# Optimization experiments

Measured on AMD Instinct MI355X. Metric: run time of the kernel, lower is better.

Reference implementation:

```python
import jax, jax.numpy as jnp
import numpy as np

NB1, NB2, B1 = 4, 4, 48
IN_F, OUT_F = 4096, 4096
BATCH = 16384


def setup_inputs() -> dict:
    key = jax.random.key(0)
    k1, k2, k3, k4 = jax.random.split(key, 4)
    i = IN_F // NB1          # 1024, per-block input width
    l = OUT_F // NB2         # 1024, per-block output width
    x = jax.random.normal(k1, (BATCH, IN_F), jnp.float32)
    # kaiming-uniform-ish scale for the factors
    w1_bfly = jax.random.normal(k2, (NB1, NB2 * B1, i), jnp.float32) * (1.0 / np.sqrt(i))
    w2_bfly = jax.random.normal(k3, (NB2, l, NB1 * B1), jnp.float32) * (1.0 / np.sqrt(NB1 * B1))
    bias = jax.random.normal(k4, (OUT_F,), jnp.float32) * 0.01
    return {"x": x, "w1_bfly": w1_bfly, "w2_bfly": w2_bfly, "bias": bias}


def reference(x, w1_bfly, w2_bfly, bias):
    # blockdiag_butterfly_multiply_einsum (Monarch-style, two block-diagonal GEMMs)
    k, q, p = w1_bfly.shape   # k = nblocks1, q = nblocks2*b1, p = in/nblocks1
    l, s, r = w2_bfly.shape   # l = nblocks2, s = out/nblocks2, r = nblocks1*b1
    b1 = q // l
    batch = x.shape[0]
    xr = x.reshape(batch, k, p)
    # stage 1: block-diagonal matmul over nblocks1
    out1 = jnp.einsum('bkp,kqp->bkq', xr, w1_bfly)               # (b, k, l*b1)
    # block transpose: (b, k, (l b1)) -> (b, l, (k b1))
    out1 = out1.reshape(batch, k, l, b1).transpose(0, 2, 1, 3).reshape(batch, l, k * b1)
    # stage 2: block-diagonal matmul over nblocks2
    out2 = jnp.einsum('blr,lsr->bls', out1, w2_bfly)             # (b, l, s)
    return out2.reshape(batch, l * s) + bias
```

## Files before the change

### kernel.cpp

```cpp
#include <hip/hip_runtime.h>
#include <cstdint>
#include <cstddef>

typedef __attribute__((ext_vector_type(8))) short short8;
typedef __attribute__((ext_vector_type(4))) float f32x4;
typedef __attribute__((ext_vector_type(4))) short short4v;

__device__ __forceinline__ unsigned short f2bf(float f) {
  unsigned u = __builtin_bit_cast(unsigned, f);
  u += 0x7fffu + ((u >> 16) & 1u);
  return (unsigned short)(u >> 16);
}

__global__ __launch_bounds__(256) void cvt_k(const float* __restrict__ src,
                                             unsigned short* __restrict__ dst, int n) {
  int i = (blockIdx.x * 256 + threadIdx.x) * 4;
  if (i + 3 < n) {
    float4 v = *(const float4*)(src + i);
    short4v o;
    o.x = (short)f2bf(v.x); o.y = (short)f2bf(v.y);
    o.z = (short)f2bf(v.z); o.w = (short)f2bf(v.w);
    *(short4v*)(dst + i) = o;
  }
}

#define S1_LDA 72
__global__ __launch_bounds__(256) void stage1_k(
    const float* __restrict__ x, const unsigned short* __restrict__ w1bf,
    unsigned short* __restrict__ Y) {
  __shared__ __attribute__((aligned(16))) unsigned short As[128 * S1_LDA];
  __shared__ __attribute__((aligned(16))) unsigned short Bs[192 * S1_LDA];
  const int t  = threadIdx.x;
  const int r0 = blockIdx.x * 128;
  const int kb = blockIdx.y;

  const int lane = t & 63;
  const int w  = t >> 6;
  const int wm = w & 1, wn = w >> 1;
  const int lm = lane & 15;
  const int lk = lane >> 4;

  const int ar = t >> 1;
  const int ac = (t & 1) * 32;
  const float* xp = x + (size_t)(r0 + ar) * 4096 + kb * 1024 + ac;
  unsigned short* asp = &As[ar * S1_LDA + ac];

  f32x4 acc[4][6];
#pragma unroll
  for (int i = 0; i < 4; ++i)
#pragma unroll
    for (int j = 0; j < 6; ++j) acc[i][j] = (f32x4)0.0f;

  for (int kt = 0; kt < 16; ++kt) {
    float4 v[8];
    const float* xq = xp + kt * 64;
#pragma unroll
    for (int i = 0; i < 8; ++i) v[i] = *(const float4*)(xq + i * 4);
#pragma unroll
    for (int i = 0; i < 4; ++i) {
      float4 a0 = v[2 * i], a1 = v[2 * i + 1];
      short8 o;
      o[0] = (short)f2bf(a0.x); o[1] = (short)f2bf(a0.y);
      o[2] = (short)f2bf(a0.z); o[3] = (short)f2bf(a0.w);
      o[4] = (short)f2bf(a1.x); o[5] = (short)f2bf(a1.y);
      o[6] = (short)f2bf(a1.z); o[7] = (short)f2bf(a1.w);
      *(short8*)(asp + i * 8) = o;
    }
#pragma unroll
    for (int i = 0; i < 6; ++i) {
      int c = t + 256 * i;
      int br = c >> 3, bs = c & 7;
      const uint4* gsrc = (const uint4*)(w1bf + (size_t)(kb * 192 + br) * 1024 + kt * 64 + bs * 8);
      *(uint4*)&Bs[br * S1_LDA + bs * 8] = *gsrc;
    }
    __syncthreads();
#pragma unroll
    for (int ks = 0; ks < 2; ++ks) {
      const int ko = ks * 32 + lk * 8;
      short8 a[4], b[6];
#pragma unroll
      for (int rt = 0; rt < 4; ++rt)
        a[rt] = *(const short8*)&As[(wm * 64 + rt * 16 + lm) * S1_LDA + ko];
#pragma unroll
      for (int ct = 0; ct < 6; ++ct)
        b[ct] = *(const short8*)&Bs[(wn * 96 + ct * 16 + lm) * S1_LDA + ko];
#pragma unroll
      for (int rt = 0; rt < 4; ++rt)
#pragma unroll
        for (int ct = 0; ct < 6; ++ct)
          acc[rt][ct] = __builtin_amdgcn_mfma_f32_16x16x32_bf16(a[rt], b[ct], acc[rt][ct], 0, 0, 0);
    }
    __syncthreads();
  }

#pragma unroll
  for (int rt = 0; rt < 4; ++rt) {
#pragma unroll
    for (int ct = 0; ct < 6; ++ct) {
      int q  = wn * 96 + ct * 16 + lm;
      int li = q / 48, j = q - li * 48;
      size_t base = (size_t)(r0 + wm * 64 + rt * 16 + lk * 4) * 768 + li * 192 + kb * 48 + j;
#pragma unroll
      for (int reg = 0; reg < 4; ++reg)
        Y[base + (size_t)reg * 768] = f2bf(acc[rt][ct][reg]);
    }
  }
}

#define S2_LDA 104
__global__ __launch_bounds__(256) void stage2_k(
    const unsigned short* __restrict__ Y, const unsigned short* __restrict__ w2bf,
    const float* __restrict__ bias, float* __restrict__ out) {
  __shared__ __attribute__((aligned(16))) unsigned short As[128 * S2_LDA];
  __shared__ __attribute__((aligned(16))) unsigned short Bs[128 * S2_LDA];
  const int t  = threadIdx.x;
  const int n0 = blockIdx.x * 128;
  const int r0 = blockIdx.y * 128;
  const int l  = blockIdx.z;

  const int lane = t & 63;
  const int w  = t >> 6;
  const int wm = w & 1, wn = w >> 1;
  const int lm = lane & 15;
  const int lk = lane >> 4;

  f32x4 acc[4][4];
#pragma unroll
  for (int i = 0; i < 4; ++i)
#pragma unroll
    for (int j = 0; j < 4; ++j) acc[i][j] = (f32x4)0.0f;

  for (int kt = 0; kt < 2; ++kt) {
#pragma unroll
    for (int i = 0; i < 6; ++i) {
      int c = t + 256 * i;
      int row = c / 12, s = c - row * 12;
      const uint4* ga = (const uint4*)(Y + (size_t)(r0 + row) * 768 + l * 192 + kt * 96 + s * 8);
      *(uint4*)&As[row * S2_LDA + s * 8] = *ga;
      const uint4* gb = (const uint4*)(w2bf + (size_t)(l * 1024 + n0 + row) * 192 + kt * 96 + s * 8);
      *(uint4*)&Bs[row * S2_LDA + s * 8] = *gb;
    }
    __syncthreads();
#pragma unroll
    for (int ks = 0; ks < 3; ++ks) {
      const int ko = ks * 32 + lk * 8;
      short8 a[4], b[4];
#pragma unroll
      for (int rt = 0; rt < 4; ++rt)
        a[rt] = *(const short8*)&As[(wm * 64 + rt * 16 + lm) * S2_LDA + ko];
#pragma unroll
      for (int ct = 0; ct < 4; ++ct)
        b[ct] = *(const short8*)&Bs[(wn * 64 + ct * 16 + lm) * S2_LDA + ko];
#pragma unroll
      for (int rt = 0; rt < 4; ++rt)
#pragma unroll
        for (int ct = 0; ct < 4; ++ct)
          acc[rt][ct] = __builtin_amdgcn_mfma_f32_16x16x32_bf16(a[rt], b[ct], acc[rt][ct], 0, 0, 0);
    }
    __syncthreads();
  }

  float bv[4];
#pragma unroll
  for (int ct = 0; ct < 4; ++ct)
    bv[ct] = bias[l * 1024 + n0 + wn * 64 + ct * 16 + lm];
#pragma unroll
  for (int rt = 0; rt < 4; ++rt) {
#pragma unroll
    for (int ct = 0; ct < 4; ++ct) {
      int n = n0 + wn * 64 + ct * 16 + lm;
      size_t base = (size_t)(r0 + wm * 64 + rt * 16 + lk * 4) * 4096 + l * 1024 + n;
#pragma unroll
      for (int reg = 0; reg < 4; ++reg)
        out[base + (size_t)reg * 4096] = acc[rt][ct][reg] + bv[ct];
    }
  }
}

extern "C" void kernel_launch(void* const* d_in, const int* in_sizes, int n_in,
                              void* d_out, int out_size, void* d_ws, size_t ws_size,
                              hipStream_t stream) {
  const float* x    = (const float*)d_in[0];
  const float* w1   = (const float*)d_in[1];
  const float* w2   = (const float*)d_in[2];
  const float* bias = (const float*)d_in[3];
  float* out = (float*)d_out;

  unsigned short* Y    = (unsigned short*)d_ws;
  unsigned short* w1bf = (unsigned short*)((char*)d_ws + 25165824);
  unsigned short* w2bf = (unsigned short*)((char*)d_ws + 25165824 + 1572864);

  cvt_k<<<768, 256, 0, stream>>>(w1, w1bf, 786432);
  cvt_k<<<768, 256, 0, stream>>>(w2, w2bf, 786432);
  stage1_k<<<dim3(128, 4), 256, 0, stream>>>(x, w1bf, Y);
  stage2_k<<<dim3(8, 128, 4), 256, 0, stream>>>(Y, w2bf, bias, out);
}
```

Baseline: 562.2 us.

## Halve stage1 row tile for more blocks and stage stage2 output through LDS

Stage1 now uses a 64-row tile with a 256x4 grid and launch bounds hinting at 4 blocks per CU. This doubles the block count from 512 (about two per CU) and cuts accumulator register use, but re-reads the w1 tile twice as often. Stage2's epilogue writes bias-added accumulators into a per-wave LDS scratch area (reusing As) and then emits coalesced float4 row stores instead of scattered scalar stores. The LDS reuse is safe because of the trailing __syncthreads in the k loop.

```diff
diff --git a/kernel.cpp b/kernel.cpp
--- a/kernel.cpp
+++ b/kernel.cpp
@@ -25,13 +25,13 @@
 }
 
 #define S1_LDA 72
-__global__ __launch_bounds__(256) void stage1_k(
+__global__ __launch_bounds__(256, 4) void stage1_k(
     const float* __restrict__ x, const unsigned short* __restrict__ w1bf,
     unsigned short* __restrict__ Y) {
-  __shared__ __attribute__((aligned(16))) unsigned short As[128 * S1_LDA];
+  __shared__ __attribute__((aligned(16))) unsigned short As[64 * S1_LDA];
   __shared__ __attribute__((aligned(16))) unsigned short Bs[192 * S1_LDA];
   const int t  = threadIdx.x;
-  const int r0 = blockIdx.x * 128;
+  const int r0 = blockIdx.x * 64;
   const int kb = blockIdx.y;
 
   const int lane = t & 63;
@@ -40,52 +40,50 @@
   const int lm = lane & 15;
   const int lk = lane >> 4;
 
-  const int ar = t >> 1;
-  const int ac = (t & 1) * 32;
-  const float* xp = x + (size_t)(r0 + ar) * 4096 + kb * 1024 + ac;
-  unsigned short* asp = &As[ar * S1_LDA + ac];
-
-  f32x4 acc[4][6];
-#pragma unroll
-  for (int i = 0; i < 4; ++i)
+  f32x4 acc[2][6];
+#pragma unroll
+  for (int i = 0; i < 2; ++i)
 #pragma unroll
     for (int j = 0; j < 6; ++j) acc[i][j] = (f32x4)0.0f;
 
+  const float* xbase = x + (size_t)r0 * 4096 + kb * 1024;
+
   for (int kt = 0; kt < 16; ++kt) {
-    float4 v[8];
-    const float* xq = xp + kt * 64;
-#pragma unroll
-    for (int i = 0; i < 8; ++i) v[i] = *(const float4*)(xq + i * 4);
-#pragma unroll
-    for (int i = 0; i < 4; ++i) {
-      float4 a0 = v[2 * i], a1 = v[2 * i + 1];
+    const float* xk = xbase + kt * 64;
+#pragma unroll
+    for (int j = 0; j < 2; ++j) {
+      int u = t + 256 * j;
+      int row = u >> 3, c8 = u & 7;
+      const float* p = xk + (size_t)row * 4096 + c8 * 8;
+      float4 a0 = *(const float4*)p;
+      float4 a1 = *(const float4*)(p + 4);
       short8 o;
       o[0] = (short)f2bf(a0.x); o[1] = (short)f2bf(a0.y);
       o[2] = (short)f2bf(a0.z); o[3] = (short)f2bf(a0.w);
       o[4] = (short)f2bf(a1.x); o[5] = (short)f2bf(a1.y);
       o[6] = (short)f2bf(a1.z); o[7] = (short)f2bf(a1.w);
-      *(short8*)(asp + i * 8) = o;
+      *(short8*)&As[row * S1_LDA + c8 * 8] = o;
     }
 #pragma unroll
     for (int i = 0; i < 6; ++i) {
       int c = t + 256 * i;
       int br = c >> 3, bs = c & 7;
-      const uint4* gsrc = (const uint4*)(w1bf + (size_t)(kb * 192 + br) * 1024 + kt * 64 + bs * 8);
-      *(uint4*)&Bs[br * S1_LDA + bs * 8] = *gsrc;
+      *(uint4*)&Bs[br * S1_LDA + bs * 8] =
+          *(const uint4*)(w1bf + (size_t)(kb * 192 + br) * 1024 + kt * 64 + bs * 8);
     }
     __syncthreads();
 #pragma unroll
     for (int ks = 0; ks < 2; ++ks) {
       const int ko = ks * 32 + lk * 8;
-      short8 a[4], b[6];
-#pragma unroll
-      for (int rt = 0; rt < 4; ++rt)
-        a[rt] = *(const short8*)&As[(wm * 64 + rt * 16 + lm) * S1_LDA + ko];
+      short8 a[2], b[6];
+#pragma unroll
+      for (int rt = 0; rt < 2; ++rt)
+        a[rt] = *(const short8*)&As[(wm * 32 + rt * 16 + lm) * S1_LDA + ko];
 #pragma unroll
       for (int ct = 0; ct < 6; ++ct)
         b[ct] = *(const short8*)&Bs[(wn * 96 + ct * 16 + lm) * S1_LDA + ko];
 #pragma unroll
-      for (int rt = 0; rt < 4; ++rt)
+      for (int rt = 0; rt < 2; ++rt)
 #pragma unroll
         for (int ct = 0; ct < 6; ++ct)
           acc[rt][ct] = __builtin_amdgcn_mfma_f32_16x16x32_bf16(a[rt], b[ct], acc[rt][ct], 0, 0, 0);
@@ -94,12 +92,12 @@
   }
 
 #pragma unroll
-  for (int rt = 0; rt < 4; ++rt) {
+  for (int rt = 0; rt < 2; ++rt) {
 #pragma unroll
     for (int ct = 0; ct < 6; ++ct) {
       int q  = wn * 96 + ct * 16 + lm;
       int li = q / 48, j = q - li * 48;
-      size_t base = (size_t)(r0 + wm * 64 + rt * 16 + lk * 4) * 768 + li * 192 + kb * 48 + j;
+      size_t base = (size_t)(r0 + wm * 32 + rt * 16 + lk * 4) * 768 + li * 192 + kb * 48 + j;
 #pragma unroll
       for (int reg = 0; reg < 4; ++reg)
         Y[base + (size_t)reg * 768] = f2bf(acc[rt][ct][reg]);
@@ -135,10 +133,10 @@
     for (int i = 0; i < 6; ++i) {
       int c = t + 256 * i;
       int row = c / 12, s = c - row * 12;
-      const uint4* ga = (const uint4*)(Y + (size_t)(r0 + row) * 768 + l * 192 + kt * 96 + s * 8);
-      *(uint4*)&As[row * S2_LDA + s * 8] = *ga;
-      const uint4* gb = (const uint4*)(w2bf + (size_t)(l * 1024 + n0 + row) * 192 + kt * 96 + s * 8);
-      *(uint4*)&Bs[row * S2_LDA + s * 8] = *gb;
+      *(uint4*)&As[row * S2_LDA + s * 8] =
+          *(const uint4*)(Y + (size_t)(r0 + row) * 768 + l * 192 + kt * 96 + s * 8);
+      *(uint4*)&Bs[row * S2_LDA + s * 8] =
+          *(const uint4*)(w2bf + (size_t)(l * 1024 + n0 + row) * 192 + kt * 96 + s * 8);
     }
     __syncthreads();
 #pragma unroll
@@ -160,19 +158,25 @@
     __syncthreads();
   }
 
+  float* LF = (float*)As + w * 1088;
   float bv[4];
 #pragma unroll
   for (int ct = 0; ct < 4; ++ct)
     bv[ct] = bias[l * 1024 + n0 + wn * 64 + ct * 16 + lm];
+
 #pragma unroll
   for (int rt = 0; rt < 4; ++rt) {
 #pragma unroll
-    for (int ct = 0; ct < 4; ++ct) {
-      int n = n0 + wn * 64 + ct * 16 + lm;
-      size_t base = (size_t)(r0 + wm * 64 + rt * 16 + lk * 4) * 4096 + l * 1024 + n;
+    for (int ct = 0; ct < 4; ++ct)
 #pragma unroll
       for (int reg = 0; reg < 4; ++reg)
-        out[base + (size_t)reg * 4096] = acc[rt][ct][reg] + bv[ct];
+        LF[(lk * 4 + reg) * 68 + ct * 16 + lm] = acc[rt][ct][reg] + bv[ct];
+#pragma unroll
+    for (int it = 0; it < 4; ++it) {
+      int idx = it * 64 + lane;
+      int rr = idx >> 4, cc = idx & 15;
+      float4 vv = *(const float4*)&LF[rr * 68 + cc * 4];
+      *(float4*)&out[(size_t)(r0 + wm * 64 + rt * 16 + rr) * 4096 + l * 1024 + n0 + wn * 64 + cc * 4] = vv;
     }
   }
 }
@@ -192,6 +196,6 @@
 
   cvt_k<<<768, 256, 0, stream>>>(w1, w1bf, 786432);
   cvt_k<<<768, 256, 0, stream>>>(w2, w2bf, 786432);
-  stage1_k<<<dim3(128, 4), 256, 0, stream>>>(x, w1bf, Y);
+  stage1_k<<<dim3(256, 4), 256, 0, stream>>>(x, w1bf, Y);
   stage2_k<<<dim3(8, 128, 4), 256, 0, stream>>>(Y, w2bf, bias, out);
 }
```

New measurement: 545.1 us. 3.0% less time.
